# Optimization experiments

Hardware: AMD Instinct MI355X
Metric: run time of the kernel (lower is better)

Reference implementation:

```python
import jax, jax.numpy as jnp
import numpy as np

NEG_INF = -1e10  # finite stand-in for -inf mask additive bias (avoids NaN on fully-masked rows)


def setup_inputs() -> dict:
    key = jax.random.key(0)
    k1, k2, k3, k4, k5 = jax.random.split(key, 5)
    B, Nq, Nkv, d = 4, 512, 512, 64
    scale = 1.0 / np.sqrt(d)
    return {
        "v_equi": jax.random.normal(k1, (B, Nkv, 3, d), dtype=jnp.float32),
        "messages": jax.random.normal(k2, (B, Nq, Nkv, d), dtype=jnp.float32),
        "adj_matrix": jax.random.randint(k3, (B, Nq, Nkv), 0, 2, dtype=jnp.int32),
        "w_coord": jax.random.normal(k4, (d, d), dtype=jnp.float32) * scale,  # torch Linear weight [out, in]
        "w_attn": jax.random.normal(k5, (d, d), dtype=jnp.float32) * scale,
    }


def reference(v_equi, messages, adj_matrix, w_coord, w_attn):
    # coord_proj: Linear without bias, y = x @ W.T
    proj_equi = jnp.einsum("bkcd,ed->bkce", v_equi, w_coord)  # [B,Nkv,3,d]
    # adj_to_attn_mask: 0 where edge exists, -inf (large negative) otherwise
    attn_mask = jnp.where(adj_matrix > 0, 0.0, NEG_INF).astype(messages.dtype)  # [B,Nq,Nkv]
    logits = messages + attn_mask[:, :, :, None]
    attn = jax.nn.softmax(logits, axis=2)  # softmax over N_kv, [B,Nq,Nkv,d]
    # batched matmul per (B, d_equi) slice: [Nq,Nkv] @ [Nkv,3]
    attn_out = jnp.einsum("bqkd,bkcd->bqcd", attn, proj_equi)  # [B,Nq,3,d]
    # L2 norm of each attention row over N_kv
    weights = jnp.sqrt(jnp.sum(attn * attn, axis=2))  # [B,Nq,d]
    attn_out = attn_out * weights[:, :, None, :]
    # attn_proj: Linear without bias
    return jnp.einsum("bqcd,ed->bqce", attn_out, w_attn)  # [B,Nq,3,d]
```

## Files before the change

kernel.cpp:

```cpp
#include <hip/hip_runtime.h>
#include <math.h>


namespace {

constexpr int kB   = 4;
constexpr int kNQ  = 512;
constexpr int kNKV = 512;
constexpr int kD   = 64;
constexpr int kQT  = 2;
constexpr float kNegInf = -1e10f;

__global__ __launch_bounds__(256)
void proj_kernel(const float* __restrict__ v, const float* __restrict__ w,
                 float* __restrict__ out) {
  __shared__ float wt[64 * 65];
  __shared__ float rows[256];
  const int t = threadIdx.x;
  for (int i = t; i < 4096; i += 256) {
    wt[(i & 63) * 65 + (i >> 6)] = w[i];
  }
  const long rowbase = (long)blockIdx.x * 4;
  rows[t] = v[rowbase * 64 + t];
  __syncthreads();
  const int r = t >> 6;
  const int e = t & 63;
  float acc = 0.f;
#pragma unroll
  for (int d = 0; d < 64; ++d) {
    acc = fmaf(rows[r * 64 + d], wt[d * 65 + e], acc);
  }
  out[rowbase * 64 + t] = acc;
}

__global__ __launch_bounds__(256)
void attn_kernel(const float* __restrict__ msg, const int* __restrict__ adj,
                 const float* __restrict__ proj, const float* __restrict__ wattn,
                 float* __restrict__ out) {
  __shared__ float wt[64 * 65];
  __shared__ float bias[kQT * kNKV];
  __shared__ float red[4][kQT][64][5];
  __shared__ float afin[kQT][3][64];

  const int t   = threadIdx.x;
  const int blk = blockIdx.x;
  const int b   = blk / (kNQ / kQT);
  const int q0  = (blk % (kNQ / kQT)) * kQT;

  for (int i = t; i < 4096; i += 256) {
    wt[(i & 63) * 65 + (i >> 6)] = wattn[i];
  }
  for (int i = t; i < kQT * kNKV; i += 256) {
    const int q = i >> 9;
    const int k = i & (kNKV - 1);
    bias[i] = (adj[((long)(b * kNQ + q0 + q)) * kNKV + k] > 0) ? 0.f : kNegInf;
  }
  __syncthreads();

  const int wave = t >> 6;
  const int lane = t & 63;
  const int ksub = lane >> 4;
  const int d0   = (lane & 15) << 2;

  const float* msg0  = msg + ((long)(b * kNQ + q0)) * kNKV * kD;
  const float* projb = proj + (long)b * kNKV * 3 * kD;

  float s[kQT][4]  = {};
  float sq[kQT][4] = {};
  float a0[kQT][4] = {};
  float a1[kQT][4] = {};
  float a2[kQT][4] = {};

#pragma unroll 4
  for (int it = 0; it < 32; ++it) {
    const int k = wave * 128 + it * 4 + ksub;
    const float4 p0 = *(const float4*)(projb + ((long)k * 3 + 0) * kD + d0);
    const float4 p1 = *(const float4*)(projb + ((long)k * 3 + 1) * kD + d0);
    const float4 p2 = *(const float4*)(projb + ((long)k * 3 + 2) * kD + d0);
#pragma unroll
    for (int j = 0; j < kQT; ++j) {
      const float4 m = *(const float4*)(msg0 + ((long)j * kNKV + k) * kD + d0);
      const float bj = bias[j * kNKV + k];
      const float e0 = __expf(m.x + bj);
      const float e1 = __expf(m.y + bj);
      const float e2 = __expf(m.z + bj);
      const float e3 = __expf(m.w + bj);
      s[j][0] += e0; s[j][1] += e1; s[j][2] += e2; s[j][3] += e3;
      sq[j][0] = fmaf(e0, e0, sq[j][0]);
      sq[j][1] = fmaf(e1, e1, sq[j][1]);
      sq[j][2] = fmaf(e2, e2, sq[j][2]);
      sq[j][3] = fmaf(e3, e3, sq[j][3]);
      a0[j][0] = fmaf(e0, p0.x, a0[j][0]);
      a0[j][1] = fmaf(e1, p0.y, a0[j][1]);
      a0[j][2] = fmaf(e2, p0.z, a0[j][2]);
      a0[j][3] = fmaf(e3, p0.w, a0[j][3]);
      a1[j][0] = fmaf(e0, p1.x, a1[j][0]);
      a1[j][1] = fmaf(e1, p1.y, a1[j][1]);
      a1[j][2] = fmaf(e2, p1.z, a1[j][2]);
      a1[j][3] = fmaf(e3, p1.w, a1[j][3]);
      a2[j][0] = fmaf(e0, p2.x, a2[j][0]);
      a2[j][1] = fmaf(e1, p2.y, a2[j][1]);
      a2[j][2] = fmaf(e2, p2.z, a2[j][2]);
      a2[j][3] = fmaf(e3, p2.w, a2[j][3]);
    }
  }

#pragma unroll
  for (int j = 0; j < kQT; ++j) {
#pragma unroll
    for (int i = 0; i < 4; ++i) {
      s[j][i]  += __shfl_xor(s[j][i], 16, 64);
      s[j][i]  += __shfl_xor(s[j][i], 32, 64);
      sq[j][i] += __shfl_xor(sq[j][i], 16, 64);
      sq[j][i] += __shfl_xor(sq[j][i], 32, 64);
      a0[j][i] += __shfl_xor(a0[j][i], 16, 64);
      a0[j][i] += __shfl_xor(a0[j][i], 32, 64);
      a1[j][i] += __shfl_xor(a1[j][i], 16, 64);
      a1[j][i] += __shfl_xor(a1[j][i], 32, 64);
      a2[j][i] += __shfl_xor(a2[j][i], 16, 64);
      a2[j][i] += __shfl_xor(a2[j][i], 32, 64);
    }
  }
  if (lane < 16) {
#pragma unroll
    for (int j = 0; j < kQT; ++j) {
#pragma unroll
      for (int i = 0; i < 4; ++i) {
        const int d = d0 + i;
        red[wave][j][d][0] = s[j][i];
        red[wave][j][d][1] = sq[j][i];
        red[wave][j][d][2] = a0[j][i];
        red[wave][j][d][3] = a1[j][i];
        red[wave][j][d][4] = a2[j][i];
      }
    }
  }
  __syncthreads();

  if (t < kQT * 64) {
    const int q = t >> 6;
    const int d = t & 63;
    float S = 0.f, SQ = 0.f, A0 = 0.f, A1 = 0.f, A2 = 0.f;
#pragma unroll
    for (int w = 0; w < 4; ++w) {
      S  += red[w][q][d][0];
      SQ += red[w][q][d][1];
      A0 += red[w][q][d][2];
      A1 += red[w][q][d][3];
      A2 += red[w][q][d][4];
    }
    const float inv = 1.f / S;
    const float wgt = sqrtf(SQ) * inv * inv;
    afin[q][0][d] = A0 * wgt;
    afin[q][1][d] = A1 * wgt;
    afin[q][2][d] = A2 * wgt;
  }
  __syncthreads();

  for (int o = t; o < kQT * 3 * 64; o += 256) {
    const int q = o / 192;
    const int c = (o % 192) / 64;
    const int e = o & 63;
    float acc = 0.f;
#pragma unroll
    for (int d = 0; d < 64; ++d) {
      acc = fmaf(afin[q][c][d], wt[d * 65 + e], acc);
    }
    out[(((long)(b * kNQ + q0 + q)) * 3 + c) * kD + e] = acc;
  }
}

}

extern "C" void kernel_launch(void* const* d_in, const int* in_sizes, int n_in,
                              void* d_out, int out_size, void* d_ws, size_t ws_size,
                              hipStream_t stream) {
  const float* v_equi   = (const float*)d_in[0];
  const float* messages = (const float*)d_in[1];
  const int*   adj      = (const int*)d_in[2];
  const float* w_coord  = (const float*)d_in[3];
  const float* w_attn   = (const float*)d_in[4];
  float* outp = (float*)d_out;
  float* projw = (float*)d_ws;

  proj_kernel<<<kB * kNKV * 3 / 4, 256, 0, stream>>>(v_equi, w_coord, projw);
  attn_kernel<<<kB * (kNQ / kQT), 256, 0, stream>>>(messages, adj, projw, w_attn, outp);
}
```

Before: 422.1 us.

## Double-buffer message loads into LDS via global_load_lds and overlay shared memory

```diff
diff --git a/kernel.cpp b/kernel.cpp
--- a/kernel.cpp
+++ b/kernel.cpp
@@ -10,6 +10,16 @@
 constexpr int kD   = 64;
 constexpr int kQT  = 2;
 constexpr float kNegInf = -1e10f;
+
+typedef float vfloat4 __attribute__((ext_vector_type(4)));
+
+typedef const __attribute__((address_space(1))) void* gas_ptr;
+typedef __attribute__((address_space(3))) void* las_ptr;
+
+__device__ __forceinline__ void gl_lds16(const float* g, float* l) {
+  __builtin_amdgcn_global_load_lds((gas_ptr)(const void*)g, (las_ptr)(void*)l,
+                                   16, 0, 0);
+}
 
 __global__ __launch_bounds__(256)
 void proj_kernel(const float* __restrict__ v, const float* __restrict__ w,
@@ -33,37 +43,48 @@
   out[rowbase * 64 + t] = acc;
 }
 
-__global__ __launch_bounds__(256)
+__global__ __launch_bounds__(256, 4)
 void attn_kernel(const float* __restrict__ msg, const int* __restrict__ adj,
                  const float* __restrict__ proj, const float* __restrict__ wattn,
                  float* __restrict__ out) {
-  __shared__ float wt[64 * 65];
+  __shared__ float smem[7104];
   __shared__ float bias[kQT * kNKV];
-  __shared__ float red[4][kQT][64][5];
-  __shared__ float afin[kQT][3][64];
+  float* const ring = smem;
+  float* const wt   = smem;
+  float* const red  = smem + 4160;
+  float* const afin = smem + 6720;
 
   const int t   = threadIdx.x;
   const int blk = blockIdx.x;
   const int b   = blk / (kNQ / kQT);
   const int q0  = (blk % (kNQ / kQT)) * kQT;
 
-  for (int i = t; i < 4096; i += 256) {
-    wt[(i & 63) * 65 + (i >> 6)] = wattn[i];
-  }
   for (int i = t; i < kQT * kNKV; i += 256) {
     const int q = i >> 9;
     const int k = i & (kNKV - 1);
     bias[i] = (adj[((long)(b * kNQ + q0 + q)) * kNKV + k] > 0) ? 0.f : kNegInf;
   }
-  __syncthreads();
 
   const int wave = t >> 6;
   const int lane = t & 63;
   const int ksub = lane >> 4;
   const int d0   = (lane & 15) << 2;
-
-  const float* msg0  = msg + ((long)(b * kNQ + q0)) * kNKV * kD;
-  const float* projb = proj + (long)b * kNKV * 3 * kD;
+  const int wbase = wave * 128;
+
+  const float* gm0 = msg + ((long)(b * kNQ + q0) * kNKV + wbase) * kD + lane * 4;
+  const float* gm1 = gm0 + (long)kNKV * kD;
+  float* const l0a = ring + ((0 * 4 + wave) * 2 + 0) * 256 + lane * 4;
+  float* const l1a = ring + ((0 * 4 + wave) * 2 + 1) * 256 + lane * 4;
+  float* const l0b = ring + ((1 * 4 + wave) * 2 + 0) * 256 + lane * 4;
+  float* const l1b = ring + ((1 * 4 + wave) * 2 + 1) * 256 + lane * 4;
+  const float* c0a = ring + ((0 * 4 + wave) * 2 + 0) * 256 + ksub * 64 + d0;
+  const float* c1a = ring + ((0 * 4 + wave) * 2 + 1) * 256 + ksub * 64 + d0;
+  const float* c0b = ring + ((1 * 4 + wave) * 2 + 0) * 256 + ksub * 64 + d0;
+  const float* c1b = ring + ((1 * 4 + wave) * 2 + 1) * 256 + ksub * 64 + d0;
+
+  const float* pp  = proj + ((long)b * kNKV + wbase + ksub) * 3 * kD + d0;
+  const float* bp0 = &bias[wbase + ksub];
+  const float* bp1 = &bias[kNKV + wbase + ksub];
 
   float s[kQT][4]  = {};
   float sq[kQT][4] = {};
@@ -71,38 +92,84 @@
   float a1[kQT][4] = {};
   float a2[kQT][4] = {};
 
-#pragma unroll 4
-  for (int it = 0; it < 32; ++it) {
-    const int k = wave * 128 + it * 4 + ksub;
-    const float4 p0 = *(const float4*)(projb + ((long)k * 3 + 0) * kD + d0);
-    const float4 p1 = *(const float4*)(projb + ((long)k * 3 + 1) * kD + d0);
-    const float4 p2 = *(const float4*)(projb + ((long)k * 3 + 2) * kD + d0);
-#pragma unroll
-    for (int j = 0; j < kQT; ++j) {
-      const float4 m = *(const float4*)(msg0 + ((long)j * kNKV + k) * kD + d0);
-      const float bj = bias[j * kNKV + k];
-      const float e0 = __expf(m.x + bj);
-      const float e1 = __expf(m.y + bj);
-      const float e2 = __expf(m.z + bj);
-      const float e3 = __expf(m.w + bj);
-      s[j][0] += e0; s[j][1] += e1; s[j][2] += e2; s[j][3] += e3;
-      sq[j][0] = fmaf(e0, e0, sq[j][0]);
-      sq[j][1] = fmaf(e1, e1, sq[j][1]);
-      sq[j][2] = fmaf(e2, e2, sq[j][2]);
-      sq[j][3] = fmaf(e3, e3, sq[j][3]);
-      a0[j][0] = fmaf(e0, p0.x, a0[j][0]);
-      a0[j][1] = fmaf(e1, p0.y, a0[j][1]);
-      a0[j][2] = fmaf(e2, p0.z, a0[j][2]);
-      a0[j][3] = fmaf(e3, p0.w, a0[j][3]);
-      a1[j][0] = fmaf(e0, p1.x, a1[j][0]);
-      a1[j][1] = fmaf(e1, p1.y, a1[j][1]);
-      a1[j][2] = fmaf(e2, p1.z, a1[j][2]);
-      a1[j][3] = fmaf(e3, p1.w, a1[j][3]);
-      a2[j][0] = fmaf(e0, p2.x, a2[j][0]);
-      a2[j][1] = fmaf(e1, p2.y, a2[j][1]);
-      a2[j][2] = fmaf(e2, p2.z, a2[j][2]);
-      a2[j][3] = fmaf(e3, p2.w, a2[j][3]);
-    }
+  auto consume = [&](const float* cm0, const float* cm1, int it,
+                     const vfloat4& P0, const vfloat4& P1, const vfloat4& P2) {
+    const vfloat4 m0 = *(const vfloat4*)cm0;
+    const vfloat4 m1 = *(const vfloat4*)cm1;
+    const float b0v = bp0[it * 4];
+    const float b1v = bp1[it * 4];
+    const float e00 = __expf(m0.x + b0v);
+    const float e01 = __expf(m0.y + b0v);
+    const float e02 = __expf(m0.z + b0v);
+    const float e03 = __expf(m0.w + b0v);
+    const float e10 = __expf(m1.x + b1v);
+    const float e11 = __expf(m1.y + b1v);
+    const float e12 = __expf(m1.z + b1v);
+    const float e13 = __expf(m1.w + b1v);
+    s[0][0] += e00; s[0][1] += e01; s[0][2] += e02; s[0][3] += e03;
+    s[1][0] += e10; s[1][1] += e11; s[1][2] += e12; s[1][3] += e13;
+    sq[0][0] = fmaf(e00, e00, sq[0][0]);
+    sq[0][1] = fmaf(e01, e01, sq[0][1]);
+    sq[0][2] = fmaf(e02, e02, sq[0][2]);
+    sq[0][3] = fmaf(e03, e03, sq[0][3]);
+    sq[1][0] = fmaf(e10, e10, sq[1][0]);
+    sq[1][1] = fmaf(e11, e11, sq[1][1]);
+    sq[1][2] = fmaf(e12, e12, sq[1][2]);
+    sq[1][3] = fmaf(e13, e13, sq[1][3]);
+    a0[0][0] = fmaf(e00, P0.x, a0[0][0]);
+    a0[0][1] = fmaf(e01, P0.y, a0[0][1]);
+    a0[0][2] = fmaf(e02, P0.z, a0[0][2]);
+    a0[0][3] = fmaf(e03, P0.w, a0[0][3]);
+    a0[1][0] = fmaf(e10, P0.x, a0[1][0]);
+    a0[1][1] = fmaf(e11, P0.y, a0[1][1]);
+    a0[1][2] = fmaf(e12, P0.z, a0[1][2]);
+    a0[1][3] = fmaf(e13, P0.w, a0[1][3]);
+    a1[0][0] = fmaf(e00, P1.x, a1[0][0]);
+    a1[0][1] = fmaf(e01, P1.y, a1[0][1]);
+    a1[0][2] = fmaf(e02, P1.z, a1[0][2]);
+    a1[0][3] = fmaf(e03, P1.w, a1[0][3]);
+    a1[1][0] = fmaf(e10, P1.x, a1[1][0]);
+    a1[1][1] = fmaf(e11, P1.y, a1[1][1]);
+    a1[1][2] = fmaf(e12, P1.z, a1[1][2]);
+    a1[1][3] = fmaf(e13, P1.w, a1[1][3]);
+    a2[0][0] = fmaf(e00, P2.x, a2[0][0]);
+    a2[0][1] = fmaf(e01, P2.y, a2[0][1]);
+    a2[0][2] = fmaf(e02, P2.z, a2[0][2]);
+    a2[0][3] = fmaf(e03, P2.w, a2[0][3]);
+    a2[1][0] = fmaf(e10, P2.x, a2[1][0]);
+    a2[1][1] = fmaf(e11, P2.y, a2[1][1]);
+    a2[1][2] = fmaf(e12, P2.z, a2[1][2]);
+    a2[1][3] = fmaf(e13, P2.w, a2[1][3]);
+  };
+
+  gl_lds16(gm0, l0a);
+  gl_lds16(gm1, l1a);
+  vfloat4 PA0 = *(const vfloat4*)(pp + 0);
+  vfloat4 PA1 = *(const vfloat4*)(pp + kD);
+  vfloat4 PA2 = *(const vfloat4*)(pp + 2 * kD);
+  vfloat4 PB0, PB1, PB2;
+
+  for (int it = 0; it < 32; it += 2) {
+    __syncthreads();
+    {
+      const int nx = it + 1;
+      gl_lds16(gm0 + nx * 256, l0b);
+      gl_lds16(gm1 + nx * 256, l1b);
+      PB0 = *(const vfloat4*)(pp + nx * 768);
+      PB1 = *(const vfloat4*)(pp + nx * 768 + kD);
+      PB2 = *(const vfloat4*)(pp + nx * 768 + 2 * kD);
+    }
+    consume(c0a, c1a, it, PA0, PA1, PA2);
+    __syncthreads();
+    if (it + 2 < 32) {
+      const int nx = it + 2;
+      gl_lds16(gm0 + nx * 256, l0a);
+      gl_lds16(gm1 + nx * 256, l1a);
+      PA0 = *(const vfloat4*)(pp + nx * 768);
+      PA1 = *(const vfloat4*)(pp + nx * 768 + kD);
+      PA2 = *(const vfloat4*)(pp + nx * 768 + 2 * kD);
+    }
+    consume(c0b, c1b, it + 1, PB0, PB1, PB2);
   }
 
 #pragma unroll
@@ -121,17 +188,24 @@
       a2[j][i] += __shfl_xor(a2[j][i], 32, 64);
     }
   }
+
+  __syncthreads();
+
+  for (int i = t; i < 4096; i += 256) {
+    wt[(i & 63) * 65 + (i >> 6)] = wattn[i];
+  }
   if (lane < 16) {
 #pragma unroll
     for (int j = 0; j < kQT; ++j) {
 #pragma unroll
       for (int i = 0; i < 4; ++i) {
         const int d = d0 + i;
-        red[wave][j][d][0] = s[j][i];
-        red[wave][j][d][1] = sq[j][i];
-        red[wave][j][d][2] = a0[j][i];
-        red[wave][j][d][3] = a1[j][i];
-        red[wave][j][d][4] = a2[j][i];
+        float* r = red + ((wave * kQT + j) * 64 + d) * 5;
+        r[0] = s[j][i];
+        r[1] = sq[j][i];
+        r[2] = a0[j][i];
+        r[3] = a1[j][i];
+        r[4] = a2[j][i];
       }
     }
   }
@@ -143,17 +217,14 @@
     float S = 0.f, SQ = 0.f, A0 = 0.f, A1 = 0.f, A2 = 0.f;
 #pragma unroll
     for (int w = 0; w < 4; ++w) {
-      S  += red[w][q][d][0];
-      SQ += red[w][q][d][1];
-      A0 += red[w][q][d][2];
-      A1 += red[w][q][d][3];
-      A2 += red[w][q][d][4];
+      const float* r = red + ((w * kQT + q) * 64 + d) * 5;
+      S += r[0]; SQ += r[1]; A0 += r[2]; A1 += r[3]; A2 += r[4];
     }
     const float inv = 1.f / S;
     const float wgt = sqrtf(SQ) * inv * inv;
-    afin[q][0][d] = A0 * wgt;
-    afin[q][1][d] = A1 * wgt;
-    afin[q][2][d] = A2 * wgt;
+    afin[(q * 3 + 0) * 64 + d] = A0 * wgt;
+    afin[(q * 3 + 1) * 64 + d] = A1 * wgt;
+    afin[(q * 3 + 2) * 64 + d] = A2 * wgt;
   }
   __syncthreads();
 
@@ -164,7 +235,7 @@
     float acc = 0.f;
 #pragma unroll
     for (int d = 0; d < 64; ++d) {
-      acc = fmaf(afin[q][c][d], wt[d * 65 + e], acc);
+      acc = fmaf(afin[(q * 3 + c) * 64 + d], wt[d * 65 + e], acc);
     }
     out[(((long)(b * kNQ + q0 + q)) * 3 + c) * kD + e] = acc;
   }
```

Result: faster. 377.8 us (-10.5%).
